# Optimization experiments

Measured on AMD Instinct MI355X. Metric: run time of the kernel, lower is better.

Reference implementation:

```python
import jax, jax.numpy as jnp
import numpy as np

EMBED_DIM = 128
NUM_HEADS = 16
D_K = EMBED_DIM // NUM_HEADS  # must equal n_wires = 8


def setup_inputs() -> dict:
    key = jax.random.key(0)
    k1, k2 = jax.random.split(key)
    x = jax.random.normal(k1, (8, 2048, EMBED_DIM), dtype=jnp.float32)
    theta = jax.random.normal(k2, (D_K,), dtype=jnp.float32)  # trainable RX angles, one per wire
    return {"x": x, "theta": theta}


def _quantum_measure(q, theta):
    # q: [B, H, S, 8]. RX(x)RX(theta) = RX(x+theta); product state gives <Z_i> = cos(phi_i).
    # CNOT chain C(0,1)..C(6,7),C(7,0) in Heisenberg picture:
    #   <Z_0> = prod_{i=1..7} cos(phi_i);  <Z_w> = prod_{i=0..w} cos(phi_i), w>=1.
    c = jnp.cos(q + theta)                       # [B,H,S,8]
    cp = jnp.cumprod(c, axis=-1)                 # prefix products prod_{0..w}
    z0 = jnp.prod(c[..., 1:], axis=-1, keepdims=True)
    return jnp.concatenate([z0, cp[..., 1:]], axis=-1)  # [B,H,S,8]


def reference(x, theta):
    B, S, E = x.shape
    # split heads: [B,S,E] -> [B,H,S,d_k]
    q = x.reshape(B, S, NUM_HEADS, D_K).transpose(0, 2, 1, 3)
    out = _quantum_measure(q, theta)             # [B,H,S,8]
    # merge heads back: [B,S,E]
    out = out.transpose(0, 2, 1, 3).reshape(B, S, E)
    scores = jnp.einsum('bse,bte->bst', out, out) / jnp.sqrt(jnp.float32(D_K))
    attn = jax.nn.softmax(scores, axis=-1)       # dropout = identity in eval mode
    return jnp.einsum('bst,bte->bse', attn, out)
```

## Files before the change

kernel.cpp:

```cpp
#include <hip/hip_runtime.h>

#define NB 8
#define SS 2048
#define DD 128
#define SCALE 0.35355339059327373f

typedef _Float16 f16x8 __attribute__((ext_vector_type(8)));
typedef float f32x16 __attribute__((ext_vector_type(16)));
typedef unsigned short u16;
typedef u16 u16x8 __attribute__((ext_vector_type(8)));

__device__ __forceinline__ unsigned pkrtz(float a, float b) {
    unsigned w;
    asm("v_cvt_pkrtz_f16_f32 %0, %1, %2" : "=v"(w) : "v"(a), "v"(b));
    return w;
}

__global__ __launch_bounds__(512) void qmeasure_kernel(const float* __restrict__ x,
                                                       const float* __restrict__ theta,
                                                       u16* __restrict__ G1,
                                                       u16* __restrict__ G2) {
    __shared__ u16 olds[32][136];
    const int bid = blockIdx.x;
    const int b = bid & 7;
    const int t = bid >> 3;
    const int tid = threadIdx.x;
    const int s = tid >> 4;
    const int c = tid & 15;

    float th[8];
    *(float4*)th = *(const float4*)theta;
    *(float4*)(th + 4) = *(const float4*)(theta + 4);

    const float* xp = x + (((size_t)b * SS + t * 32 + s) * DD) + c * 8;
    float4 a = *(const float4*)xp;
    float4 a2 = *(const float4*)(xp + 4);
    float cc[8];
    cc[0] = __cosf(a.x + th[0]);  cc[1] = __cosf(a.y + th[1]);
    cc[2] = __cosf(a.z + th[2]);  cc[3] = __cosf(a.w + th[3]);
    cc[4] = __cosf(a2.x + th[4]); cc[5] = __cosf(a2.y + th[5]);
    cc[6] = __cosf(a2.z + th[6]); cc[7] = __cosf(a2.w + th[7]);
    float o[8];
    o[1] = cc[0] * cc[1];
    o[2] = o[1] * cc[2]; o[3] = o[2] * cc[3]; o[4] = o[3] * cc[4];
    o[5] = o[4] * cc[5]; o[6] = o[5] * cc[6]; o[7] = o[6] * cc[7];
    float z = cc[1] * cc[2]; z *= cc[3]; z *= cc[4]; z *= cc[5]; z *= cc[6]; z *= cc[7];
    o[0] = z;

    u16x8 w;
#pragma unroll
    for (int e = 0; e < 8; ++e) w[e] = __builtin_bit_cast(u16, (_Float16)o[e]);
    *(u16x8*)&olds[s][c * 8] = w;
    __syncthreads();

    {
        const int kc = tid >> 6, hh = (tid >> 5) & 1, r = tid & 31;
        u16x8 g;
#pragma unroll
        for (int u = 0; u < 8; ++u) g[u] = olds[r][kc * 16 + hh * 8 + u];
        *(u16x8*)(G1 + (size_t)b * (SS * DD) + ((size_t)t * 512 + tid) * 8) = g;
    }
    {
        const int lo5 = tid & 31;
        const int hh = (tid >> 5) & 1;
        const int dkc = tid >> 6;
        const int dt = dkc >> 1, kc2 = dkc & 1;
        u16x8 g;
#pragma unroll
        for (int u = 0; u < 8; ++u) g[u] = olds[kc2 * 16 + hh * 8 + u][dt * 32 + lo5];
        const int chunk = t * 512 + dkc * 64 + hh * 32 + lo5;
        *(u16x8*)(G2 + (size_t)b * (SS * DD) + (size_t)chunk * 8) = g;
    }
}

__global__ __launch_bounds__(512, 2) void qattn_kernel(const u16* __restrict__ G1g,
                                                       const u16* __restrict__ G2g,
                                                       float* __restrict__ out) {
    __shared__ __align__(16) u16 sb[2][2][4][4096];

    const int tid = threadIdx.x;
    const int lane = tid & 63;
    const int wave = tid >> 6;
    const int lo5 = lane & 31;
    const int hi = lane >> 5;
    const int qw = wave & 1;
    const int kq = wave >> 1;
    const int bid = blockIdx.x;
    const int b = bid & 7;
    const int qg = bid >> 3;

    const u16* G1b = G1g + (size_t)b * (SS * DD);
    const u16* G2b = G2g + (size_t)b * (SS * DD);
    const u16* sbase = (qw ? G2b : G1b);

    f16x8 qf[8];
    {
        const u16* qp = G1b + (size_t)(qg * 2 + qw) * 4096 + lane * 8;
#pragma unroll
        for (int kc = 0; kc < 8; ++kc) qf[kc] = *(const f16x8*)(qp + kc * 512);
    }

    f32x16 accT[4];
#pragma unroll
    for (int dt = 0; dt < 4; ++dt)
#pragma unroll
        for (int e = 0; e < 16; ++e) accT[dt][e] = 0.f;
    float m = -3.0e38f, l = 0.f;

    f16x8 sreg[8];
    {
        const u16* src = sbase + (size_t)(kq * 16) * 4096 + lane * 8;
#pragma unroll
        for (int w = 0; w < 8; ++w) sreg[w] = *(const f16x8*)(src + w * 512);
        u16* dst = &sb[0][qw][kq][0] + lane * 8;
#pragma unroll
        for (int w = 0; w < 8; ++w) *(f16x8*)(dst + w * 512) = sreg[w];
        const u16* src1 = sbase + (size_t)(kq * 16 + 1) * 4096 + lane * 8;
#pragma unroll
        for (int w = 0; w < 8; ++w) sreg[w] = *(const f16x8*)(src1 + w * 512);
    }
    asm volatile("s_waitcnt lgkmcnt(0)" ::: "memory");
    __builtin_amdgcn_sched_barrier(0);
    __builtin_amdgcn_s_barrier();

    for (int it = 0; it < 16; ++it) {
        const int cur = it & 1;
        if (it >= 1) {
        }
        if (it < 15) {
            u16* dst = &sb[cur ^ 1][qw][kq][0] + lane * 8;
#pragma unroll
            for (int w = 0; w < 8; ++w) *(f16x8*)(dst + w * 512) = sreg[w];
            if (it < 14) {
                const u16* src = sbase + (size_t)(kq * 16 + it + 2) * 4096 + lane * 8;
#pragma unroll
                for (int w = 0; w < 8; ++w) sreg[w] = *(const f16x8*)(src + w * 512);
            }
            asm volatile("s_waitcnt lgkmcnt(0)" ::: "memory");
            __builtin_amdgcn_sched_barrier(0);
        }
        __builtin_amdgcn_s_barrier();
        __builtin_amdgcn_sched_barrier(0);

        const u16* Kb = &sb[cur][0][kq][0] + lane * 8;
        const u16* Vb = &sb[cur][1][kq][0] + lane * 8;

        f32x16 acc;
#pragma unroll
        for (int e = 0; e < 16; ++e) acc[e] = 0.f;
        __builtin_amdgcn_s_setprio(1);
#pragma unroll
        for (int kc = 0; kc < 8; ++kc) {
            f16x8 kf = *(const f16x8*)(Kb + kc * 512);
            acc = __builtin_amdgcn_mfma_f32_32x32x16_f16(kf, qf[kc], acc, 0, 0, 0);
        }
        __builtin_amdgcn_s_setprio(0);

        float ma = fmaxf(fmaxf(acc[0], acc[1]), acc[2]);
        float mb = fmaxf(fmaxf(acc[8], acc[9]), acc[10]);
        ma = fmaxf(fmaxf(ma, acc[3]), acc[4]);
        mb = fmaxf(fmaxf(mb, acc[11]), acc[12]);
        ma = fmaxf(fmaxf(ma, acc[5]), acc[6]);
        mb = fmaxf(fmaxf(mb, acc[13]), acc[14]);
        ma = fmaxf(fmaxf(ma, acc[7]), mb);
        float tmax = fmaxf(ma, acc[15]) * SCALE;
        tmax = fmaxf(tmax, __shfl_xor(tmax, 32));
        if (!__all(tmax <= m + 8.f)) {
            const float mnew = fmaxf(m, tmax);
            const float corr = __expf(m - mnew);
            l *= corr;
#pragma unroll
            for (int dt = 0; dt < 4; ++dt)
#pragma unroll
                for (int e = 0; e < 16; ++e) accT[dt][e] *= corr;
            m = mnew;
        }
#pragma unroll
        for (int r = 0; r < 16; ++r) acc[r] = __expf(acc[r] * SCALE - m);
        float s0 = (acc[0] + acc[1]) + (acc[2] + acc[3]);
        float s1 = (acc[4] + acc[5]) + (acc[6] + acc[7]);
        float s2 = (acc[8] + acc[9]) + (acc[10] + acc[11]);
        float s3 = (acc[12] + acc[13]) + (acc[14] + acc[15]);
        float rowsum = (s0 + s1) + (s2 + s3);
        rowsum += __shfl_xor(rowsum, 32);
        l += rowsum;

        f16x8 pa[2];
#pragma unroll
        for (int kc2 = 0; kc2 < 2; ++kc2) {
            const int r0 = kc2 * 8;
            unsigned w0 = pkrtz(acc[r0 + 0], acc[r0 + 1]);
            unsigned w2 = pkrtz(acc[r0 + 4], acc[r0 + 5]);
            asm("v_permlane32_swap_b32 %0, %1" : "+v"(w0), "+v"(w2));
            unsigned w1 = pkrtz(acc[r0 + 2], acc[r0 + 3]);
            unsigned w3 = pkrtz(acc[r0 + 6], acc[r0 + 7]);
            asm("v_permlane32_swap_b32 %0, %1" : "+v"(w1), "+v"(w3));
            union { unsigned w[4]; f16x8 v; } u;
            u.w[0] = w0; u.w[1] = w1; u.w[2] = w2; u.w[3] = w3;
            pa[kc2] = u.v;
        }

        __builtin_amdgcn_s_setprio(1);
#pragma unroll
        for (int dt = 0; dt < 4; ++dt) {
            f32x16 a = accT[dt];
#pragma unroll
            for (int kc2 = 0; kc2 < 2; ++kc2) {
                f16x8 vf = *(const f16x8*)(Vb + (dt * 2 + kc2) * 512);
                a = __builtin_amdgcn_mfma_f32_32x32x16_f16(vf, pa[kc2], a, 0, 0, 0);
            }
            accT[dt] = a;
        }
        __builtin_amdgcn_s_setprio(0);

        __builtin_amdgcn_sched_barrier(0);
        __builtin_amdgcn_s_barrier();
    }

    __syncthreads();
    float* obuf = (float*)(&sb[0][0][0][0]);
    float* mlb = (float*)((unsigned char*)(&sb[0][0][0][0]) + 49152);
    float* orow = out + ((size_t)b * SS + qg * 64 + qw * 32 + lo5) * DD;
#pragma unroll
    for (int half = 0; half < 2; ++half) {
        if (kq > 0) {
            if (half == 0 && hi == 0) {
                mlb[((qw * 3 + (kq - 1)) * 2 + 0) * 32 + lo5] = m;
                mlb[((qw * 3 + (kq - 1)) * 2 + 1) * 32 + lo5] = l;
            }
#pragma unroll
            for (int dh = 0; dh < 2; ++dh)
#pragma unroll
                for (int r = 0; r < 16; ++r)
                    obuf[(((qw * 3 + (kq - 1)) * 2 + dh) * 16 + r) * 64 + lane] =
                        accT[half * 2 + dh][r];
        }
        __syncthreads();
        if (kq == 0) {
            const float mj0 = mlb[((qw * 3 + 0) * 2 + 0) * 32 + lo5];
            const float lj0 = mlb[((qw * 3 + 0) * 2 + 1) * 32 + lo5];
            const float mj1 = mlb[((qw * 3 + 1) * 2 + 0) * 32 + lo5];
            const float lj1 = mlb[((qw * 3 + 1) * 2 + 1) * 32 + lo5];
            const float mj2 = mlb[((qw * 3 + 2) * 2 + 0) * 32 + lo5];
            const float lj2 = mlb[((qw * 3 + 2) * 2 + 1) * 32 + lo5];
            const float ms = fmaxf(fmaxf(m, mj0), fmaxf(mj1, mj2));
            const float w0 = __expf(m - ms), w1 = __expf(mj0 - ms);
            const float w2 = __expf(mj1 - ms), w3 = __expf(mj2 - ms);
            const float linv = 1.f / (l * w0 + lj0 * w1 + lj1 * w2 + lj2 * w3);
#pragma unroll
            for (int dh = 0; dh < 2; ++dh) {
                const int dt = half * 2 + dh;
#pragma unroll
                for (int r = 0; r < 16; ++r) {
                    const float o = accT[dt][r] * w0 +
                                    obuf[(((qw * 3 + 0) * 2 + dh) * 16 + r) * 64 + lane] * w1 +
                                    obuf[(((qw * 3 + 1) * 2 + dh) * 16 + r) * 64 + lane] * w2 +
                                    obuf[(((qw * 3 + 2) * 2 + dh) * 16 + r) * 64 + lane] * w3;
                    const int drow = (r & 3) + 8 * (r >> 2) + 4 * hi;
                    orow[dt * 32 + drow] = o * linv;
                }
            }
        }
        __syncthreads();
    }
}

extern "C" void kernel_launch(void* const* d_in, const int* in_sizes, int n_in,
                              void* d_out, int out_size, void* d_ws, size_t ws_size,
                              hipStream_t stream) {
    const float* x = (const float*)d_in[0];
    const float* theta = (const float*)d_in[1];
    float* outp = (float*)d_out;
    u16* G1 = (u16*)d_ws;
    u16* G2 = G1 + (size_t)NB * SS * DD;

    qmeasure_kernel<<<512, 512, 0, stream>>>(x, theta, G1, G2);
    qattn_kernel<<<256, 512, 0, stream>>>(G1, G2, outp);
}
```

Baseline: 40.16 us.

## Stream K/V tiles directly into LDS with async global_load_lds double buffering

Result: no change. 40.66 us (+1.2%).

```diff
diff --git a/kernel.cpp b/kernel.cpp
--- a/kernel.cpp
+++ b/kernel.cpp
@@ -3,17 +3,25 @@
 #define NB 8
 #define SS 2048
 #define DD 128
-#define SCALE 0.35355339059327373f
+#define SCALE2 0.5101817664764817f
+#define NEGINF -3.0e38f
 
 typedef _Float16 f16x8 __attribute__((ext_vector_type(8)));
 typedef float f32x16 __attribute__((ext_vector_type(16)));
 typedef unsigned short u16;
 typedef u16 u16x8 __attribute__((ext_vector_type(8)));
-
-__device__ __forceinline__ unsigned pkrtz(float a, float b) {
-    unsigned w;
+typedef unsigned int u32;
+
+__device__ __forceinline__ u32 pkrtz(float a, float b) {
+    u32 w;
     asm("v_cvt_pkrtz_f16_f32 %0, %1, %2" : "=v"(w) : "v"(a), "v"(b));
     return w;
+}
+
+__device__ __forceinline__ void gload_lds16(const u16* g, u16* l) {
+    __builtin_amdgcn_global_load_lds(
+        (const __attribute__((address_space(1))) unsigned*)g,
+        (__attribute__((address_space(3))) unsigned*)l, 16, 0, 0);
 }
 
 __global__ __launch_bounds__(512) void qmeasure_kernel(const float* __restrict__ x,
@@ -100,61 +108,52 @@
         for (int kc = 0; kc < 8; ++kc) qf[kc] = *(const f16x8*)(qp + kc * 512);
     }
 
+#pragma unroll
+    for (int pb = 0; pb < 2; ++pb) {
+        const u16* src = sbase + (size_t)(kq * 16 + pb) * 4096 + lane * 8;
+        u16* dst = &sb[pb][qw][kq][0];
+#pragma unroll
+        for (int w = 0; w < 8; ++w) gload_lds16(src + w * 512, dst + w * 512);
+    }
+
     f32x16 accT[4];
 #pragma unroll
     for (int dt = 0; dt < 4; ++dt)
 #pragma unroll
         for (int e = 0; e < 16; ++e) accT[dt][e] = 0.f;
-    float m = -3.0e38f, l = 0.f;
-
-    f16x8 sreg[8];
-    {
-        const u16* src = sbase + (size_t)(kq * 16) * 4096 + lane * 8;
-#pragma unroll
-        for (int w = 0; w < 8; ++w) sreg[w] = *(const f16x8*)(src + w * 512);
-        u16* dst = &sb[0][qw][kq][0] + lane * 8;
-#pragma unroll
-        for (int w = 0; w < 8; ++w) *(f16x8*)(dst + w * 512) = sreg[w];
-        const u16* src1 = sbase + (size_t)(kq * 16 + 1) * 4096 + lane * 8;
-#pragma unroll
-        for (int w = 0; w < 8; ++w) sreg[w] = *(const f16x8*)(src1 + w * 512);
-    }
-    asm volatile("s_waitcnt lgkmcnt(0)" ::: "memory");
-    __builtin_amdgcn_sched_barrier(0);
-    __builtin_amdgcn_s_barrier();
+    float m = NEGINF, l = 0.f;
 
     for (int it = 0; it < 16; ++it) {
         const int cur = it & 1;
-        if (it >= 1) {
-        }
-        if (it < 15) {
-            u16* dst = &sb[cur ^ 1][qw][kq][0] + lane * 8;
-#pragma unroll
-            for (int w = 0; w < 8; ++w) *(f16x8*)(dst + w * 512) = sreg[w];
-            if (it < 14) {
-                const u16* src = sbase + (size_t)(kq * 16 + it + 2) * 4096 + lane * 8;
-#pragma unroll
-                for (int w = 0; w < 8; ++w) sreg[w] = *(const f16x8*)(src + w * 512);
-            }
-            asm volatile("s_waitcnt lgkmcnt(0)" ::: "memory");
-            __builtin_amdgcn_sched_barrier(0);
-        }
+        if (it < 15) asm volatile("s_waitcnt vmcnt(8)" ::: "memory");
+        else         asm volatile("s_waitcnt vmcnt(0)" ::: "memory");
+        __builtin_amdgcn_sched_barrier(0);
         __builtin_amdgcn_s_barrier();
         __builtin_amdgcn_sched_barrier(0);
 
         const u16* Kb = &sb[cur][0][kq][0] + lane * 8;
         const u16* Vb = &sb[cur][1][kq][0] + lane * 8;
 
-        f32x16 acc;
-#pragma unroll
-        for (int e = 0; e < 16; ++e) acc[e] = 0.f;
+        f32x16 acA, acB;
+#pragma unroll
+        for (int e = 0; e < 16; ++e) { acA[e] = 0.f; acB[e] = 0.f; }
         __builtin_amdgcn_s_setprio(1);
 #pragma unroll
-        for (int kc = 0; kc < 8; ++kc) {
+        for (int kc = 0; kc < 4; ++kc) {
             f16x8 kf = *(const f16x8*)(Kb + kc * 512);
-            acc = __builtin_amdgcn_mfma_f32_32x32x16_f16(kf, qf[kc], acc, 0, 0, 0);
+            acA = __builtin_amdgcn_mfma_f32_32x32x16_f16(kf, qf[kc], acA, 0, 0, 0);
+        }
+#pragma unroll
+        for (int kc = 4; kc < 8; ++kc) {
+            f16x8 kf = *(const f16x8*)(Kb + kc * 512);
+            acB = __builtin_amdgcn_mfma_f32_32x32x16_f16(kf, qf[kc], acB, 0, 0, 0);
         }
         __builtin_amdgcn_s_setprio(0);
+        f32x16 acc = acA + acB;
+
+        f16x8 vf[8];
+#pragma unroll
+        for (int j = 0; j < 8; ++j) vf[j] = *(const f16x8*)(Vb + j * 512);
 
         float ma = fmaxf(fmaxf(acc[0], acc[1]), acc[2]);
         float mb = fmaxf(fmaxf(acc[8], acc[9]), acc[10]);
@@ -163,11 +162,11 @@
         ma = fmaxf(fmaxf(ma, acc[5]), acc[6]);
         mb = fmaxf(fmaxf(mb, acc[13]), acc[14]);
         ma = fmaxf(fmaxf(ma, acc[7]), mb);
-        float tmax = fmaxf(ma, acc[15]) * SCALE;
+        float tmax = fmaxf(ma, acc[15]) * SCALE2;
         tmax = fmaxf(tmax, __shfl_xor(tmax, 32));
         if (!__all(tmax <= m + 8.f)) {
             const float mnew = fmaxf(m, tmax);
-            const float corr = __expf(m - mnew);
+            const float corr = exp2f(m - mnew);
             l *= corr;
 #pragma unroll
             for (int dt = 0; dt < 4; ++dt)
@@ -176,7 +175,7 @@
             m = mnew;
         }
 #pragma unroll
-        for (int r = 0; r < 16; ++r) acc[r] = __expf(acc[r] * SCALE - m);
+        for (int r = 0; r < 16; ++r) acc[r] = exp2f(acc[r] * SCALE2 - m);
         float s0 = (acc[0] + acc[1]) + (acc[2] + acc[3]);
         float s1 = (acc[4] + acc[5]) + (acc[6] + acc[7]);
         float s2 = (acc[8] + acc[9]) + (acc[10] + acc[11]);
@@ -189,13 +188,13 @@
 #pragma unroll
         for (int kc2 = 0; kc2 < 2; ++kc2) {
             const int r0 = kc2 * 8;
-            unsigned w0 = pkrtz(acc[r0 + 0], acc[r0 + 1]);
-            unsigned w2 = pkrtz(acc[r0 + 4], acc[r0 + 5]);
+            u32 w0 = pkrtz(acc[r0 + 0], acc[r0 + 1]);
+            u32 w2 = pkrtz(acc[r0 + 4], acc[r0 + 5]);
             asm("v_permlane32_swap_b32 %0, %1" : "+v"(w0), "+v"(w2));
-            unsigned w1 = pkrtz(acc[r0 + 2], acc[r0 + 3]);
-            unsigned w3 = pkrtz(acc[r0 + 6], acc[r0 + 7]);
+            u32 w1 = pkrtz(acc[r0 + 2], acc[r0 + 3]);
+            u32 w3 = pkrtz(acc[r0 + 6], acc[r0 + 7]);
             asm("v_permlane32_swap_b32 %0, %1" : "+v"(w1), "+v"(w3));
-            union { unsigned w[4]; f16x8 v; } u;
+            union { u32 w[4]; f16x8 v; } u;
             u.w[0] = w0; u.w[1] = w1; u.w[2] = w2; u.w[3] = w3;
             pa[kc2] = u.v;
         }
@@ -204,17 +203,23 @@
 #pragma unroll
         for (int dt = 0; dt < 4; ++dt) {
             f32x16 a = accT[dt];
-#pragma unroll
-            for (int kc2 = 0; kc2 < 2; ++kc2) {
-                f16x8 vf = *(const f16x8*)(Vb + (dt * 2 + kc2) * 512);
-                a = __builtin_amdgcn_mfma_f32_32x32x16_f16(vf, pa[kc2], a, 0, 0, 0);
-            }
+            a = __builtin_amdgcn_mfma_f32_32x32x16_f16(vf[dt * 2 + 0], pa[0], a, 0, 0, 0);
+            a = __builtin_amdgcn_mfma_f32_32x32x16_f16(vf[dt * 2 + 1], pa[1], a, 0, 0, 0);
             accT[dt] = a;
         }
         __builtin_amdgcn_s_setprio(0);
 
+        asm volatile("s_waitcnt lgkmcnt(0)" ::: "memory");
         __builtin_amdgcn_sched_barrier(0);
         __builtin_amdgcn_s_barrier();
+        __builtin_amdgcn_sched_barrier(0);
+
+        if (it < 14) {
+            const u16* src = sbase + (size_t)(kq * 16 + it + 2) * 4096 + lane * 8;
+            u16* dst = &sb[cur][qw][kq][0];
+#pragma unroll
+            for (int w = 0; w < 8; ++w) gload_lds16(src + w * 512, dst + w * 512);
+        }
     }
 
     __syncthreads();
@@ -244,8 +249,8 @@
             const float mj2 = mlb[((qw * 3 + 2) * 2 + 0) * 32 + lo5];
             const float lj2 = mlb[((qw * 3 + 2) * 2 + 1) * 32 + lo5];
             const float ms = fmaxf(fmaxf(m, mj0), fmaxf(mj1, mj2));
-            const float w0 = __expf(m - ms), w1 = __expf(mj0 - ms);
-            const float w2 = __expf(mj1 - ms), w3 = __expf(mj2 - ms);
+            const float w0 = exp2f(m - ms), w1 = exp2f(mj0 - ms);
+            const float w2 = exp2f(mj1 - ms), w3 = exp2f(mj2 - ms);
             const float linv = 1.f / (l * w0 + lj0 * w1 + lj1 * w2 + lj2 * w3);
 #pragma unroll
             for (int dh = 0; dh < 2; ++dh) {
```
